# Performance work log

Hardware: AMD Instinct MI355X
Metric: run time of the kernel (lower is better)

## Reference

```python
import jax, jax.numpy as jnp
import numpy as np


def pixel_coordinates(h, w):
    # (h, w, 2) grid of (x, y) in [-1, 1]
    y = jnp.linspace(-1.0, 1.0, h)
    x = jnp.linspace(-1.0, 1.0, w)
    yy, xx = jnp.meshgrid(y, x, indexing='ij')
    return jnp.stack([xx, yy], axis=-1)


def base_grid(h_in, w_in):
    y = jnp.linspace(-1.0 + 1.0 / h_in, 1.0 - 1.0 / h_in, h_in)
    x = jnp.linspace(-1.0 + 1.0 / w_in, 1.0 - 1.0 / w_in, w_in)
    yy, xx = jnp.meshgrid(y, x, indexing='ij')
    return jnp.stack([xx, yy], axis=-1)  # [h_in, w_in, 2]


def setup_inputs() -> dict:
    key = jax.random.key(0)
    params = jax.random.normal(key, (2, 9, 32, 32), dtype=jnp.float32)
    return {"params": params, "h_out": 128, "w_out": 128}


def reference(params, h_out, w_out):
    B, _, h_in, w_in = params.shape
    N = h_in * w_in
    p = jnp.transpose(params, (0, 2, 3, 1))  # [B, h_in, w_in, 9]

    # positions (mu): base grid + tanh(offset) * (2/h_in)
    mu = base_grid(h_in, w_in)[None] + jnp.tanh(p[..., 0:2]) * (2.0 / h_in)
    mu = mu.reshape(B, N, 2)

    # covariance via Cholesky-like factor L = [[exp(a), 0], [b, exp(c)]]
    v1x = jnp.exp(p[..., 2])
    v2x = p[..., 3]
    v2y = jnp.exp(p[..., 4])
    zero = jnp.zeros_like(v1x)
    L = jnp.stack([jnp.stack([v1x, zero], axis=-1),
                   jnp.stack([v2x, v2y], axis=-1)], axis=-2)  # [B,h,w,2,2]
    cov = L @ jnp.swapaxes(L, -1, -2)
    cov = cov.reshape(B, N, 2, 2) + jnp.eye(2, dtype=params.dtype) * 1e-5
    Sigma_inv = jnp.linalg.inv(cov)  # [B, N, 2, 2]

    colors = jax.nn.sigmoid(p[..., 5:8]).reshape(B, N, 3)
    opacities = jax.nn.sigmoid(p[..., 8]).reshape(B, N)

    coords = pixel_coordinates(h_out, w_out)  # [H, W, 2]
    dx = coords[None, None] - mu[:, :, None, None, :]  # [B, N, H, W, 2]
    exponent = -0.5 * jnp.einsum('bnhwi,bnij,bnhwj->bnhw', dx, Sigma_inv, dx)
    exponent = jnp.clip(exponent, -20.0, 20.0)
    kernel = jnp.exp(exponent)  # [B, N, H, W]

    weights = opacities[:, :, None, None] * kernel
    weights_sum = jnp.sum(weights, axis=1, keepdims=True) + 1e-8
    norm_w = weights / weights_sum  # [B, N, H, W]
    image = jnp.einsum('bnhw,bnc->bchw', norm_w, colors)  # [B, 3, H, W]
    return image
```

## Files before the change

kernel.cpp:

```cpp
#include <hip/hip_runtime.h>


#define NB   2
#define NG   1024
#define HOUT 128
#define WOUT 128
#define GSTRIDE 12

__global__ __launch_bounds__(256) void gauss_setup(const float* __restrict__ params,
                                                   float* __restrict__ gd) {
    int gid = blockIdx.x * blockDim.x + threadIdx.x;
    if (gid >= NB * NG) return;
    int b = gid >> 10;
    int n = gid & (NG - 1);
    int h = n >> 5;
    int w = n & 31;

    const float* P = params + b * 9 * NG + n;
    float p0 = P[0 * NG];
    float p1 = P[1 * NG];
    float p2 = P[2 * NG];
    float p3 = P[3 * NG];
    float p4 = P[4 * NG];
    float p5 = P[5 * NG];
    float p6 = P[6 * NG];
    float p7 = P[7 * NG];
    float p8 = P[8 * NG];

    float mux = -0.96875f + (float)w * 0.0625f + tanhf(p0) * 0.0625f;
    float muy = -0.96875f + (float)h * 0.0625f + tanhf(p1) * 0.0625f;

    float ea  = expf(p2);
    float ec  = expf(p4);
    float c00 = ea * ea + 1e-5f;
    float c01 = p3 * ea;
    float c11 = p3 * p3 + ec * ec + 1e-5f;
    float det = c00 * c11 - c01 * c01;
    float id  = 1.0f / det;
    float Sa  =  c11 * id;
    float Sb  = -c01 * id;
    float Sc  =  c00 * id;

    const float s = -0.72134752044448169f;
    float A  = s * Sa;
    float B2 = 2.0f * s * Sb;
    float C  = s * Sc;

    float cr = 1.0f / (1.0f + expf(-p5));
    float cg = 1.0f / (1.0f + expf(-p6));
    float cb = 1.0f / (1.0f + expf(-p7));
    float op = 1.0f / (1.0f + expf(-p8));

    float* o = gd + gid * GSTRIDE;
    o[0]  = mux;  o[1]  = muy;  o[2]  = A;       o[3]  = B2;
    o[4]  = C;    o[5]  = op;   o[6]  = op * cr; o[7]  = op * cg;
    o[8]  = op * cb; o[9] = 0.0f; o[10] = 0.0f; o[11] = 0.0f;
}

__global__ __launch_bounds__(512) void gauss_render(const float* __restrict__ gd,
                                                    float* __restrict__ out) {
    __shared__ float4 sred[512];

    const int tx  = threadIdx.x;
    const int ty  = threadIdx.y;
    const int tid = ty * 64 + tx;
    const int blk = blockIdx.x;
    const int b   = blk >> 8;
    const int pix = ((blk & 255) << 6) + tx;

    const int h = pix >> 7;
    const int w = pix & 127;
    const float px = -1.0f + (float)w * (2.0f / 127.0f);
    const float py = -1.0f + (float)h * (2.0f / 127.0f);

    const int chunk = __builtin_amdgcn_readfirstlane(ty);
    const float* __restrict__ gp =
        gd + (size_t)b * NG * GSTRIDE + (size_t)chunk * (NG / 8) * GSTRIDE;

    float wsum = 0.0f, ar = 0.0f, ag = 0.0f, ab = 0.0f;

    #pragma unroll 4
    for (int j = 0; j < NG / 8; ++j) {
        const float* __restrict__ r = gp + j * GSTRIDE;
        const float mux = r[0], muy = r[1];
        const float A   = r[2], B2  = r[3], C = r[4];
        const float op  = r[5], ocr = r[6], ocg = r[7], ocb = r[8];

        float dx = px - mux;
        float dy = py - muy;
        float m  = A * dx;
        m        = fmaf(B2, dy, m);
        float e2 = fmaf(C * dy, dy, m * dx);
        e2 = fmaxf(e2, -28.853900817779268f);
        float k = __builtin_amdgcn_exp2f(e2);

        wsum = fmaf(op,  k, wsum);
        ar   = fmaf(ocr, k, ar);
        ag   = fmaf(ocg, k, ag);
        ab   = fmaf(ocb, k, ab);
    }

    sred[tid] = make_float4(wsum, ar, ag, ab);
    __syncthreads();

    if (ty == 0) {
        float4 a = sred[tx];
        #pragma unroll
        for (int k2 = 1; k2 < 8; ++k2) {
            float4 t = sred[k2 * 64 + tx];
            a.x += t.x; a.y += t.y; a.z += t.z; a.w += t.w;
        }
        float inv = 1.0f / (a.x + 1e-8f);
        float* ob = out + b * 3 * (HOUT * WOUT) + pix;
        ob[0]                 = a.y * inv;
        ob[HOUT * WOUT]       = a.z * inv;
        ob[2 * HOUT * WOUT]   = a.w * inv;
    }
}

extern "C" void kernel_launch(void* const* d_in, const int* in_sizes, int n_in,
                              void* d_out, int out_size, void* d_ws, size_t ws_size,
                              hipStream_t stream) {
    const float* params = (const float*)d_in[0];
    float* gd  = (float*)d_ws;
    float* out = (float*)d_out;

    hipLaunchKernelGGL(gauss_setup, dim3((NB * NG + 255) / 256), dim3(256), 0, stream,
                       params, gd);
    hipLaunchKernelGGL(gauss_render, dim3(NB * (HOUT * WOUT) / 64), dim3(64, 8), 0,
                       stream, gd, out);
}
```

Baseline: 74.52 us.

## Interleave gaussian pairs for packed float2 math and split over 16 chunks

Setup now writes gaussians in pairs, with each field of two gaussians stored side by side. The render loop can then load v2f values and use packed FP32 operations (v_pk_fma/v_pk_mul) that handle two gaussians per instruction. The render block grows to 64x16 threads, so each thread handles 32 gaussian pairs, and the shared-memory reduction sums 16 partials. Packed math cuts the VALU instruction count, though exp2 is still scalar. The larger blocks use more LDS and add reduction work, and occupancy may change.

```diff
diff --git a/kernel.cpp b/kernel.cpp
--- a/kernel.cpp
+++ b/kernel.cpp
@@ -5,7 +5,10 @@
 #define NG   1024
 #define HOUT 128
 #define WOUT 128
-#define GSTRIDE 12
+#define PSTRIDE 24
+#define NCHUNK 16
+
+typedef float v2f __attribute__((ext_vector_type(2)));
 
 __global__ __launch_bounds__(256) void gauss_setup(const float* __restrict__ params,
                                                    float* __restrict__ gd) {
@@ -51,15 +54,15 @@
     float cb = 1.0f / (1.0f + expf(-p7));
     float op = 1.0f / (1.0f + expf(-p8));
 
-    float* o = gd + gid * GSTRIDE;
-    o[0]  = mux;  o[1]  = muy;  o[2]  = A;       o[3]  = B2;
-    o[4]  = C;    o[5]  = op;   o[6]  = op * cr; o[7]  = op * cg;
-    o[8]  = op * cb; o[9] = 0.0f; o[10] = 0.0f; o[11] = 0.0f;
+    float* o = gd + ((size_t)b * (NG / 2) + (n >> 1)) * PSTRIDE + (n & 1);
+    o[0]  = mux;  o[2]  = muy;  o[4]  = A;       o[6]  = B2;
+    o[8]  = C;    o[10] = op;   o[12] = op * cr; o[14] = op * cg;
+    o[16] = op * cb;
 }
 
-__global__ __launch_bounds__(512) void gauss_render(const float* __restrict__ gd,
-                                                    float* __restrict__ out) {
-    __shared__ float4 sred[512];
+__global__ __launch_bounds__(1024, 8) void gauss_render(const float* __restrict__ gd,
+                                                        float* __restrict__ out) {
+    __shared__ float4 sred[1024];
 
     const int tx  = threadIdx.x;
     const int ty  = threadIdx.y;
@@ -72,49 +75,56 @@
     const int w = pix & 127;
     const float px = -1.0f + (float)w * (2.0f / 127.0f);
     const float py = -1.0f + (float)h * (2.0f / 127.0f);
+    const v2f px2 = {px, px};
+    const v2f py2 = {py, py};
 
     const int chunk = __builtin_amdgcn_readfirstlane(ty);
-    const float* __restrict__ gp =
-        gd + (size_t)b * NG * GSTRIDE + (size_t)chunk * (NG / 8) * GSTRIDE;
+    const v2f* __restrict__ gp = (const v2f*)(gd
+        + (size_t)b * (NG / 2) * PSTRIDE
+        + (size_t)chunk * (NG / 2 / NCHUNK) * PSTRIDE);
 
-    float wsum = 0.0f, ar = 0.0f, ag = 0.0f, ab = 0.0f;
+    v2f wsum2 = {0.0f, 0.0f}, ar2 = {0.0f, 0.0f};
+    v2f ag2   = {0.0f, 0.0f}, ab2 = {0.0f, 0.0f};
 
-    #pragma unroll 4
-    for (int j = 0; j < NG / 8; ++j) {
-        const float* __restrict__ r = gp + j * GSTRIDE;
-        const float mux = r[0], muy = r[1];
-        const float A   = r[2], B2  = r[3], C = r[4];
-        const float op  = r[5], ocr = r[6], ocg = r[7], ocb = r[8];
+    #pragma unroll 2
+    for (int j = 0; j < NG / 2 / NCHUNK; ++j) {
+        const v2f* __restrict__ r = gp + j * (PSTRIDE / 2);
+        v2f mux2 = r[0], muy2 = r[1];
+        v2f A2   = r[2], B22  = r[3], C2 = r[4];
+        v2f op2  = r[5], ocr2 = r[6], ocg2 = r[7], ocb2 = r[8];
 
-        float dx = px - mux;
-        float dy = py - muy;
-        float m  = A * dx;
-        m        = fmaf(B2, dy, m);
-        float e2 = fmaf(C * dy, dy, m * dx);
-        e2 = fmaxf(e2, -28.853900817779268f);
-        float k = __builtin_amdgcn_exp2f(e2);
+        v2f dx = px2 - mux2;
+        v2f dy = py2 - muy2;
+        v2f m  = A2 * dx;
+        m      = __builtin_elementwise_fma(B22, dy, m);
+        v2f t  = C2 * dy;
+        v2f e2 = __builtin_elementwise_fma(t, dy, m * dx);
+        e2 = __builtin_elementwise_max(e2, (v2f){-28.853900817779268f,
+                                                 -28.853900817779268f});
+        v2f k2 = {__builtin_amdgcn_exp2f(e2.x), __builtin_amdgcn_exp2f(e2.y)};
 
-        wsum = fmaf(op,  k, wsum);
-        ar   = fmaf(ocr, k, ar);
-        ag   = fmaf(ocg, k, ag);
-        ab   = fmaf(ocb, k, ab);
+        wsum2 = __builtin_elementwise_fma(op2,  k2, wsum2);
+        ar2   = __builtin_elementwise_fma(ocr2, k2, ar2);
+        ag2   = __builtin_elementwise_fma(ocg2, k2, ag2);
+        ab2   = __builtin_elementwise_fma(ocb2, k2, ab2);
     }
 
-    sred[tid] = make_float4(wsum, ar, ag, ab);
+    sred[tid] = make_float4(wsum2.x + wsum2.y, ar2.x + ar2.y,
+                            ag2.x + ag2.y,     ab2.x + ab2.y);
     __syncthreads();
 
     if (ty == 0) {
         float4 a = sred[tx];
         #pragma unroll
-        for (int k2 = 1; k2 < 8; ++k2) {
-            float4 t = sred[k2 * 64 + tx];
+        for (int k2i = 1; k2i < NCHUNK; ++k2i) {
+            float4 t = sred[k2i * 64 + tx];
             a.x += t.x; a.y += t.y; a.z += t.z; a.w += t.w;
         }
         float inv = 1.0f / (a.x + 1e-8f);
         float* ob = out + b * 3 * (HOUT * WOUT) + pix;
-        ob[0]                 = a.y * inv;
-        ob[HOUT * WOUT]       = a.z * inv;
-        ob[2 * HOUT * WOUT]   = a.w * inv;
+        ob[0]               = a.y * inv;
+        ob[HOUT * WOUT]     = a.z * inv;
+        ob[2 * HOUT * WOUT] = a.w * inv;
     }
 }
 
@@ -127,6 +137,6 @@
 
     hipLaunchKernelGGL(gauss_setup, dim3((NB * NG + 255) / 256), dim3(256), 0, stream,
                        params, gd);
-    hipLaunchKernelGGL(gauss_render, dim3(NB * (HOUT * WOUT) / 64), dim3(64, 8), 0,
+    hipLaunchKernelGGL(gauss_render, dim3(NB * (HOUT * WOUT) / 64), dim3(64, 16), 0,
                        stream, gd, out);
 }
```

Measured after the change: 71.06 us. 1.05x faster.
